# Optimization experiments

Measured on AMD Instinct MI355X. Metric: run time of the kernel, lower is better.

## Reference

```python
import jax, jax.numpy as jnp
import numpy as np

D_MODEL = 2048
N_HEADS = 32
N_KV_HEADS = 8
HEAD_DIM = D_MODEL // N_HEADS
N_REP = N_HEADS // N_KV_HEADS
ROPE_BASE = 10000.0


def _rope_tables(seq_len, dim, dtype):
    inv_freq = 1.0 / (ROPE_BASE ** (jnp.arange(0, dim, 2, dtype=jnp.float32) / dim))
    t = jnp.arange(seq_len, dtype=jnp.float32)
    freqs = jnp.einsum('i,j->ij', t, inv_freq)          # [S, dim/2]
    emb = jnp.concatenate([freqs, freqs], axis=-1)      # [S, dim]
    return jnp.cos(emb).astype(dtype), jnp.sin(emb).astype(dtype)


def _apply_rotation(x, cos, sin):
    # x: [B, H, S, D]; cos/sin: [S, D] broadcast over B,H
    half = x.shape[-1] // 2
    x1, x2 = x[..., :half], x[..., half:]
    rot = jnp.concatenate([-x2, x1], axis=-1)
    return rot * sin + x * cos


def setup_inputs() -> dict:
    key = jax.random.key(0)
    kx, kq, kk, kv, ko = jax.random.split(key, 5)
    B, S = 2, 2048
    scale_in = 1.0 / np.sqrt(D_MODEL)
    x = jax.random.normal(kx, (B, S, D_MODEL), dtype=jnp.float32)
    Wq = jax.random.normal(kq, (N_HEADS * HEAD_DIM, D_MODEL), dtype=jnp.float32) * scale_in
    Wk = jax.random.normal(kk, (N_KV_HEADS * HEAD_DIM, D_MODEL), dtype=jnp.float32) * scale_in
    Wv = jax.random.normal(kv, (N_KV_HEADS * HEAD_DIM, D_MODEL), dtype=jnp.float32) * scale_in
    Wo = jax.random.normal(ko, (D_MODEL, N_HEADS * HEAD_DIM), dtype=jnp.float32) * scale_in
    # additive causal mask, broadcast over batch and heads
    neg = jnp.float32(-1e9)
    causal = jnp.triu(jnp.full((S, S), neg, dtype=jnp.float32), k=1)[None, None]
    return {"x": x, "Wq": Wq, "Wk": Wk, "Wv": Wv, "Wo": Wo, "mask": causal}


def reference(x, Wq, Wk, Wv, Wo, mask):
    B, S, _ = x.shape
    q = (x @ Wq.T).reshape(B, S, N_HEADS, HEAD_DIM).transpose(0, 2, 1, 3)      # [B,H,S,D]
    k = (x @ Wk.T).reshape(B, S, N_KV_HEADS, HEAD_DIM).transpose(0, 2, 1, 3)   # [B,Hkv,S,D]
    v = (x @ Wv.T).reshape(B, S, N_KV_HEADS, HEAD_DIM).transpose(0, 2, 1, 3)
    cos, sin = _rope_tables(S, HEAD_DIM, x.dtype)
    q = _apply_rotation(q, cos, sin)
    k = _apply_rotation(k, cos, sin)
    # repeat_kv: [B,Hkv,S,D] -> [B,Hkv*n_rep,S,D]
    k = jnp.repeat(k, N_REP, axis=1)
    v = jnp.repeat(v, N_REP, axis=1)
    scale = jnp.sqrt(jnp.float32(HEAD_DIM)).astype(x.dtype)
    scores = jnp.einsum('bhqd,bhkd->bhqk', q, k) / scale
    scores = scores + mask
    attn = jax.nn.softmax(scores.astype(jnp.float32), axis=-1).astype(q.dtype)
    out = jnp.einsum('bhqk,bhkd->bhqd', attn, v)
    out = out.transpose(0, 2, 1, 3).reshape(B, S, N_HEADS * HEAD_DIM)
    return out @ Wo.T
```

## Files before the change

kernel.cpp:

```cpp
#include <hip/hip_runtime.h>


typedef __bf16 bf16x8 __attribute__((ext_vector_type(8)));
typedef __bf16 bf16x4 __attribute__((ext_vector_type(4)));
typedef float f32x4 __attribute__((ext_vector_type(4)));

__device__ inline f32x4 mfma16(bf16x8 a, bf16x8 b, f32x4 c) {
    return __builtin_amdgcn_mfma_f32_16x16x32_bf16(a, b, c, 0, 0, 0);
}

__device__ inline void gld16(const __bf16* g, __bf16* l) {
    __builtin_amdgcn_global_load_lds(
        (const __attribute__((address_space(1))) void*)g,
        (__attribute__((address_space(3))) void*)l, 16, 0, 0);
}

__device__ inline bf16x4 pk4(float a, float b, float c, float d) {
    bf16x4 r; r[0] = (__bf16)a; r[1] = (__bf16)b; r[2] = (__bf16)c; r[3] = (__bf16)d;
    return r;
}

#define SCALE_Q 0.18033688011112042f
#define L2IF    0.4152410118609203f
#define INV2PI  0.15915494309189535f

__global__ void cvt4_kernel(const float* __restrict__ x,  const float* __restrict__ wq,
                            const float* __restrict__ wk, const float* __restrict__ wv,
                            __bf16* __restrict__ xb, __bf16* __restrict__ wqkvb)
{
    int i = blockIdx.x * blockDim.x + threadIdx.x;
    const float* src; __bf16* dst;
    if (i < 2097152)      { src = x  + (size_t)i * 4;  dst = xb + (size_t)i * 4; }
    else if (i < 3145728) { int j = i - 2097152; src = wq + (size_t)j * 4; dst = wqkvb + (size_t)j * 4; }
    else if (i < 3407872) { int j = i - 3145728; src = wk + (size_t)j * 4; dst = wqkvb + 4194304 + (size_t)j * 4; }
    else                  { int j = i - 3407872; src = wv + (size_t)j * 4; dst = wqkvb + 5242880 + (size_t)j * 4; }
    float4 f = *(const float4*)src;
    *(bf16x4*)dst = pk4(f.x, f.y, f.z, f.w);
}

__global__ void cvt_kernel(const float* __restrict__ in, __bf16* __restrict__ out, int n4)
{
    int i = blockIdx.x * blockDim.x + threadIdx.x;
    if (i >= n4) return;
    float4 f = ((const float4*)in)[i];
    ((bf16x4*)out)[i] = pk4(f.x, f.y, f.z, f.w);
}

template<bool ROPE, bool OUT_F32>
__global__ __launch_bounds__(512, 2) void gemm256(
    const __bf16* __restrict__ A, const __bf16* __restrict__ Bw,
    void* __restrict__ Cv, int M, int N, int K)
{
    __shared__ __bf16 LA[2][16384];
    __shared__ __bf16 LB[2][16384];
    const int tid  = threadIdx.x;
    const int lane = tid & 63;
    const int w    = tid >> 6;
    const int lm   = lane & 15;
    const int quad = lane >> 4;
    const int wr   = w >> 2;
    const int wc   = w & 3;

    int bx, by;
    {
        int nwg = gridDim.x * gridDim.y;
        int id  = blockIdx.x + gridDim.x * blockIdx.y;
        int q   = nwg >> 3;
        int swz = (id & 7) * q + (id >> 3);
        by = swz / gridDim.x;
        bx = swz - by * gridDim.x;
    }
    const int m0 = by * 256;
    const int n0 = bx * 256;
    const int NT = K >> 6;

    const int srow = tid >> 3;
    const int scol = ((tid & 7) ^ (srow & 7)) * 8;
    const int ldst = tid * 8;
    const __bf16* ga = A  + (size_t)(m0 + srow) * K + scol;
    const __bf16* gb = Bw + (size_t)(n0 + srow) * K + scol;

    auto STA = [&](int bf, int r, int u) {
        gld16(ga + (size_t)r * K + u * 64, &LA[bf][r * 64 + ldst]);
    };
    auto STB = [&](int bf, int r, int u) {
        gld16(gb + (size_t)r * K + u * 64, &LB[bf][r * 64 + ldst]);
    };

    f32x4 acc[8][4];
    #pragma unroll
    for (int i = 0; i < 8; ++i)
        #pragma unroll
        for (int j = 0; j < 4; ++j)
            acc[i][j] = (f32x4){0.f, 0.f, 0.f, 0.f};

    const int axo = (wr * 128 + lm) * 64;
    const int bxo = (wc * 64  + lm) * 64;
    const int ks0 = ((quad * 8)      ^ ((lm & 7) * 8));
    const int ks1 = ((32 + quad * 8) ^ ((lm & 7) * 8));

    STA(0, 0, 0); STA(0, 64, 0); STA(0, 128, 0); STA(0, 192, 0);
    STB(0, 0, 0); STB(0, 64, 0); STB(0, 128, 0); STB(0, 192, 0);
    STA(1, 0, 1); STA(1, 128, 1); STB(1, 0, 1); STA(1, 64, 1); STB(1, 64, 1);
    asm volatile("s_waitcnt vmcnt(5)" ::: "memory");
    __builtin_amdgcn_s_barrier();
    asm volatile("" ::: "memory");

    bf16x8 Af[4][2], Bf[4][2];
    for (int t = 0; t < NT; ++t) {
        const int b = t & 1;
        const __bf16* la = LA[b];
        const __bf16* lb = LB[b];
        #pragma unroll
        for (int mi = 0; mi < 4; ++mi) {
            Af[mi][0] = *(const bf16x8*)(la + axo + mi * 1024 + ks0);
            Af[mi][1] = *(const bf16x8*)(la + axo + mi * 1024 + ks1);
        }
        #pragma unroll
        for (int ni = 0; ni < 2; ++ni) {
            Bf[ni][0] = *(const bf16x8*)(lb + bxo + ni * 1024 + ks0);
            Bf[ni][1] = *(const bf16x8*)(lb + bxo + ni * 1024 + ks1);
        }
        if (t + 1 < NT) { STA(b ^ 1, 192, t + 1); STB(b ^ 1, 128, t + 1); }
        __builtin_amdgcn_s_barrier();
        asm volatile("s_waitcnt lgkmcnt(0)" ::: "memory");
        __builtin_amdgcn_s_setprio(1);
        #pragma unroll
        for (int mi = 0; mi < 4; ++mi)
            #pragma unroll
            for (int ni = 0; ni < 2; ++ni) {
                acc[mi][ni] = mfma16(Af[mi][0], Bf[ni][0], acc[mi][ni]);
                acc[mi][ni] = mfma16(Af[mi][1], Bf[ni][1], acc[mi][ni]);
            }
        __builtin_amdgcn_s_setprio(0);
        __builtin_amdgcn_s_barrier();
        #pragma unroll
        for (int ni = 2; ni < 4; ++ni) {
            Bf[ni][0] = *(const bf16x8*)(lb + bxo + ni * 1024 + ks0);
            Bf[ni][1] = *(const bf16x8*)(lb + bxo + ni * 1024 + ks1);
        }
        if (t + 1 < NT) STB(b ^ 1, 192, t + 1);
        if (t + 2 < NT) STA(b, 0, t + 2);
        __builtin_amdgcn_s_barrier();
        asm volatile("s_waitcnt lgkmcnt(0)" ::: "memory");
        __builtin_amdgcn_s_setprio(1);
        #pragma unroll
        for (int mi = 0; mi < 4; ++mi)
            #pragma unroll
            for (int ni = 2; ni < 4; ++ni) {
                acc[mi][ni] = mfma16(Af[mi][0], Bf[ni][0], acc[mi][ni]);
                acc[mi][ni] = mfma16(Af[mi][1], Bf[ni][1], acc[mi][ni]);
            }
        __builtin_amdgcn_s_setprio(0);
        __builtin_amdgcn_s_barrier();
        #pragma unroll
        for (int mi = 0; mi < 4; ++mi) {
            Af[mi][0] = *(const bf16x8*)(la + axo + (mi + 4) * 1024 + ks0);
            Af[mi][1] = *(const bf16x8*)(la + axo + (mi + 4) * 1024 + ks1);
        }
        if (t + 2 < NT) { STA(b, 128, t + 2); STB(b, 0, t + 2); }
        __builtin_amdgcn_s_barrier();
        asm volatile("s_waitcnt lgkmcnt(0)" ::: "memory");
        __builtin_amdgcn_s_setprio(1);
        #pragma unroll
        for (int mi = 0; mi < 4; ++mi)
            #pragma unroll
            for (int ni = 0; ni < 2; ++ni) {
                acc[mi + 4][ni] = mfma16(Af[mi][0], Bf[ni][0], acc[mi + 4][ni]);
                acc[mi + 4][ni] = mfma16(Af[mi][1], Bf[ni][1], acc[mi + 4][ni]);
            }
        __builtin_amdgcn_s_setprio(0);
        __builtin_amdgcn_s_barrier();
        if (t + 2 < NT) { STA(b, 64, t + 2); STB(b, 64, t + 2); }
        __builtin_amdgcn_s_barrier();
        __builtin_amdgcn_s_setprio(1);
        #pragma unroll
        for (int mi = 0; mi < 4; ++mi)
            #pragma unroll
            for (int ni = 2; ni < 4; ++ni) {
                acc[mi + 4][ni] = mfma16(Af[mi][0], Bf[ni][0], acc[mi + 4][ni]);
                acc[mi + 4][ni] = mfma16(Af[mi][1], Bf[ni][1], acc[mi + 4][ni]);
            }
        __builtin_amdgcn_s_setprio(0);
        if (t < NT - 2)       asm volatile("s_waitcnt vmcnt(5)" ::: "memory");
        else if (t == NT - 2) asm volatile("s_waitcnt vmcnt(0)" ::: "memory");
        __builtin_amdgcn_s_barrier();
        asm volatile("" ::: "memory");
    }

    float sc = 1.0f;
    if (ROPE) {
        const int colbase = n0 + wc * 64;
        const int region  = (colbase < 2048) ? 0 : (colbase < 2560 ? 1 : 2);
        if (region < 2) {
            if (region == 0) sc = SCALE_Q;
            float invr[2];
            invr[0] = exp2f(-(float)lm        * L2IF) * INV2PI;
            invr[1] = exp2f(-(float)(16 + lm) * L2IF) * INV2PI;
            #pragma unroll
            for (int i = 0; i < 8; ++i)
                #pragma unroll
                for (int r = 0; r < 4; ++r) {
                    float tt = (float)((m0 + wr * 128 + i * 16 + quad * 4 + r) & 2047);
                    #pragma unroll
                    for (int jp = 0; jp < 2; ++jp) {
                        float aR = tt * invr[jp];
                        aR -= floorf(aR);
                        float cs = __builtin_amdgcn_cosf(aR);
                        float sn = __builtin_amdgcn_sinf(aR);
                        float x1 = acc[i][jp][r], x2 = acc[i][jp + 2][r];
                        acc[i][jp][r]     = x1 * cs - x2 * sn;
                        acc[i][jp + 2][r] = x2 * cs + x1 * sn;
                    }
                }
        }
    }

    #pragma unroll
    for (int i = 0; i < 8; ++i)
        #pragma unroll
        for (int j = 0; j < 4; ++j)
            #pragma unroll
            for (int r = 0; r < 4; ++r) {
                int row = m0 + wr * 128 + i * 16 + quad * 4 + r;
                int col = n0 + wc * 64 + j * 16 + lm;
                if (OUT_F32)
                    ((float*)Cv)[(size_t)row * N + col] = acc[i][j][r];
                else
                    ((__bf16*)Cv)[(size_t)row * N + col] = (__bf16)(acc[i][j][r] * sc);
            }
}

__global__ __launch_bounds__(512, 2) void gemm_o(
    const __bf16* __restrict__ A, const __bf16* __restrict__ Bw,
    float* __restrict__ C, int M, int N, int K)
{
    __shared__ __bf16 LA[2][16384];
    __shared__ __bf16 LB[2][8192];
    const int tid  = threadIdx.x;
    const int lane = tid & 63;
    const int w    = tid >> 6;
    const int lm   = lane & 15;
    const int quad = lane >> 4;
    const int wr   = w >> 1;
    const int wc   = w & 1;

    int bx, by;
    {
        int id  = blockIdx.x + gridDim.x * blockIdx.y;
        int swz = (id & 7) * 32 + (id >> 3);
        by = swz >> 4;
        bx = swz & 15;
    }
    const int m0 = by * 256;
    const int n0 = bx * 128;
    const int NT = K >> 6;

    const int srow = tid >> 3;
    const int scol = ((tid & 7) ^ (srow & 7)) * 8;
    const int ldst = tid * 8;
    const __bf16* ga = A  + (size_t)(m0 + srow) * K + scol;
    const __bf16* gb = Bw + (size_t)(n0 + srow) * K + scol;

    auto STA = [&](int bf, int r, int u) {
        gld16(ga + (size_t)r * K + u * 64, &LA[bf][r * 64 + ldst]);
    };
    auto STB = [&](int bf, int r, int u) {
        gld16(gb + (size_t)r * K + u * 64, &LB[bf][r * 64 + ldst]);
    };

    f32x4 acc[4][4];
    #pragma unroll
    for (int i = 0; i < 4; ++i)
        #pragma unroll
        for (int j = 0; j < 4; ++j)
            acc[i][j] = (f32x4){0.f, 0.f, 0.f, 0.f};

    const int axo = (wr * 64 + lm) * 64;
    const int bxo = (wc * 64 + lm) * 64;
    const int ks0 = ((quad * 8)      ^ ((lm & 7) * 8));
    const int ks1 = ((32 + quad * 8) ^ ((lm & 7) * 8));

    STA(0, 0, 0); STA(0, 64, 0); STA(0, 128, 0); STA(0, 192, 0);
    STB(0, 0, 0); STB(0, 64, 0);
    STA(1, 0, 1); STA(1, 64, 1); STA(1, 128, 1); STA(1, 192, 1);
    STB(1, 0, 1); STB(1, 64, 1);
    asm volatile("s_waitcnt vmcnt(6)" ::: "memory");
    __builtin_amdgcn_s_barrier();
    asm volatile("" ::: "memory");

    bf16x8 Af[4][2], Bf[4][2];
    for (int t = 0; t < NT; ++t) {
        const int b = t & 1;
        const __bf16* la = LA[b];
        const __bf16* lb = LB[b];
        #pragma unroll
        for (int mi = 0; mi < 2; ++mi) {
            Af[mi][0] = *(const bf16x8*)(la + axo + mi * 1024 + ks0);
            Af[mi][1] = *(const bf16x8*)(la + axo + mi * 1024 + ks1);
        }
        #pragma unroll
        for (int ni = 0; ni < 2; ++ni) {
            Bf[ni][0] = *(const bf16x8*)(lb + bxo + ni * 1024 + ks0);
            Bf[ni][1] = *(const bf16x8*)(lb + bxo + ni * 1024 + ks1);
        }
        __builtin_amdgcn_s_barrier();
        asm volatile("s_waitcnt lgkmcnt(0)" ::: "memory");
        __builtin_amdgcn_s_setprio(1);
        #pragma unroll
        for (int mi = 0; mi < 2; ++mi)
            #pragma unroll
            for (int ni = 0; ni < 2; ++ni) {
                acc[mi][ni] = mfma16(Af[mi][0], Bf[ni][0], acc[mi][ni]);
                acc[mi][ni] = mfma16(Af[mi][1], Bf[ni][1], acc[mi][ni]);
            }
        __builtin_amdgcn_s_setprio(0);
        __builtin_amdgcn_s_barrier();
        #pragma unroll
        for (int ni = 2; ni < 4; ++ni) {
            Bf[ni][0] = *(const bf16x8*)(lb + bxo + ni * 1024 + ks0);
            Bf[ni][1] = *(const bf16x8*)(lb + bxo + ni * 1024 + ks1);
        }
        __builtin_amdgcn_s_barrier();
        asm volatile("s_waitcnt lgkmcnt(0)" ::: "memory");
        __builtin_amdgcn_s_setprio(1);
        #pragma unroll
        for (int mi = 0; mi < 2; ++mi)
            #pragma unroll
            for (int ni = 2; ni < 4; ++ni) {
                acc[mi][ni] = mfma16(Af[mi][0], Bf[ni][0], acc[mi][ni]);
                acc[mi][ni] = mfma16(Af[mi][1], Bf[ni][1], acc[mi][ni]);
            }
        __builtin_amdgcn_s_setprio(0);
        __builtin_amdgcn_s_barrier();
        #pragma unroll
        for (int mi = 2; mi < 4; ++mi) {
            Af[mi][0] = *(const bf16x8*)(la + axo + mi * 1024 + ks0);
            Af[mi][1] = *(const bf16x8*)(la + axo + mi * 1024 + ks1);
        }
        if (t + 2 < NT) { STB(b, 0, t + 2); STB(b, 64, t + 2); }
        __builtin_amdgcn_s_barrier();
        asm volatile("s_waitcnt lgkmcnt(0)" ::: "memory");
        __builtin_amdgcn_s_setprio(1);
        #pragma unroll
        for (int mi = 2; mi < 4; ++mi)
            #pragma unroll
            for (int ni = 0; ni < 2; ++ni) {
                acc[mi][ni] = mfma16(Af[mi][0], Bf[ni][0], acc[mi][ni]);
                acc[mi][ni] = mfma16(Af[mi][1], Bf[ni][1], acc[mi][ni]);
            }
        __builtin_amdgcn_s_setprio(0);
        __builtin_amdgcn_s_barrier();
        if (t + 2 < NT) {
            STA(b, 0, t + 2); STA(b, 64, t + 2);
            STA(b, 128, t + 2); STA(b, 192, t + 2);
        }
        __builtin_amdgcn_s_setprio(1);
        #pragma unroll
        for (int mi = 2; mi < 4; ++mi)
            #pragma unroll
            for (int ni = 2; ni < 4; ++ni) {
                acc[mi][ni] = mfma16(Af[mi][0], Bf[ni][0], acc[mi][ni]);
                acc[mi][ni] = mfma16(Af[mi][1], Bf[ni][1], acc[mi][ni]);
            }
        __builtin_amdgcn_s_setprio(0);
        if (t < NT - 2) asm volatile("s_waitcnt vmcnt(6)" ::: "memory");
        else            asm volatile("s_waitcnt vmcnt(0)" ::: "memory");
        __builtin_amdgcn_s_barrier();
        asm volatile("" ::: "memory");
    }

    #pragma unroll
    for (int i = 0; i < 4; ++i)
        #pragma unroll
        for (int j = 0; j < 4; ++j)
            #pragma unroll
            for (int r = 0; r < 4; ++r) {
                int row = m0 + wr * 64 + i * 16 + quad * 4 + r;
                int col = n0 + wc * 64 + j * 16 + lm;
                C[(size_t)row * N + col] = acc[i][j][r];
            }
}

__global__ __launch_bounds__(256) void transpose_kernel(
    const __bf16* __restrict__ in, __bf16* __restrict__ out, int rowstride)
{
    __shared__ __bf16 T[64][72];
    const int t0 = blockIdx.x * 64;
    const int d0 = blockIdx.y * 64;
    const int r = threadIdx.x >> 2, c = (threadIdx.x & 3) * 16;
    *(int4*)&T[r][c]     = *(const int4*)(in + (size_t)(t0 + r) * rowstride + d0 + c);
    *(int4*)&T[r][c + 8] = *(const int4*)(in + (size_t)(t0 + r) * rowstride + d0 + c + 8);
    __syncthreads();
    bf16x8 o0, o1;
    #pragma unroll
    for (int i = 0; i < 8; ++i) { o0[i] = T[c + i][r]; o1[i] = T[c + 8 + i][r]; }
    *(bf16x8*)(out + (size_t)(d0 + r) * 4096 + t0 + c)     = o0;
    *(bf16x8*)(out + (size_t)(d0 + r) * 4096 + t0 + c + 8) = o1;
}

#define RS  64
#define PKS 64

__device__ inline void attn_tile(
    const bf16x8 (&qf)[2], f32x4 (&oacc)[4], float& l,
    int qbase, int k0, int w, int lm, int quad,
    const __bf16* Ks, const __bf16* Vs, __bf16* Ptw)
{
    const int kb0 = (quad ^ (lm & 7)) * 8;
    const int kb1 = ((quad + 4) ^ (lm & 7)) * 8;
    f32x4 st[4];
    #pragma unroll
    for (int n = 0; n < 4; ++n)
        st[n] = (f32x4){0.f, 0.f, 0.f, 0.f};

    #pragma unroll
    for (int n = 0; n < 4; ++n) {
        bf16x8 kf0 = *(const bf16x8*)&Ks[(n * 16 + lm) * RS + kb0];
        bf16x8 kf1 = *(const bf16x8*)&Ks[(n * 16 + lm) * RS + kb1];
        st[n] = mfma16(kf0, qf[0], st[n]);
        st[n] = mfma16(kf1, qf[1], st[n]);
    }

    const int qi = qbase + w * 16 + lm;
    const bool any_mask = (k0 + 63 > qbase + w * 16);
    #pragma unroll
    for (int n = 0; n < 4; ++n) {
        const int kv0 = k0 + n * 16 + quad * 4;
        float e0, e1, e2, e3;
        if (any_mask) {
            e0 = (kv0     > qi) ? 0.f : __builtin_amdgcn_exp2f(st[n][0]);
            e1 = (kv0 + 1 > qi) ? 0.f : __builtin_amdgcn_exp2f(st[n][1]);
            e2 = (kv0 + 2 > qi) ? 0.f : __builtin_amdgcn_exp2f(st[n][2]);
            e3 = (kv0 + 3 > qi) ? 0.f : __builtin_amdgcn_exp2f(st[n][3]);
        } else {
            e0 = __builtin_amdgcn_exp2f(st[n][0]); e1 = __builtin_amdgcn_exp2f(st[n][1]);
            e2 = __builtin_amdgcn_exp2f(st[n][2]); e3 = __builtin_amdgcn_exp2f(st[n][3]);
        }
        l += (e0 + e1) + (e2 + e3);
        *(bf16x4*)&Ptw[lm * PKS + ((n * 4 + quad) ^ ((lm & 7) << 1)) * 4] =
            pk4(e0, e1, e2, e3);
    }

    bf16x8 pf0 = *(const bf16x8*)&Ptw[lm * PKS + kb0];
    bf16x8 pf1 = *(const bf16x8*)&Ptw[lm * PKS + kb1];
    #pragma unroll
    for (int dt = 0; dt < 4; ++dt) {
        bf16x8 vf0 = *(const bf16x8*)&Vs[(dt * 16 + lm) * RS + kb0];
        bf16x8 vf1 = *(const bf16x8*)&Vs[(dt * 16 + lm) * RS + kb1];
        oacc[dt] = mfma16(vf0, pf0, oacc[dt]);
        oacc[dt] = mfma16(vf1, pf1, oacc[dt]);
    }
}

__device__ inline void attn_tile2(
    const bf16x8 (&qfA)[2], const bf16x8 (&qfB)[2],
    f32x4 (&oA)[4], f32x4 (&oB)[4], float& lA, float& lB,
    int qbA, int k0, int w, int lm, int quad,
    const __bf16* Ks, const __bf16* Vs, __bf16* PtA, __bf16* PtB)
{
    const int kb0 = (quad ^ (lm & 7)) * 8;
    const int kb1 = ((quad + 4) ^ (lm & 7)) * 8;
    f32x4 stA[4], stB[4];
    #pragma unroll
    for (int n = 0; n < 4; ++n) {
        stA[n] = (f32x4){0.f, 0.f, 0.f, 0.f};
        stB[n] = (f32x4){0.f, 0.f, 0.f, 0.f};
    }

    #pragma unroll
    for (int n = 0; n < 4; ++n) {
        bf16x8 kf0 = *(const bf16x8*)&Ks[(n * 16 + lm) * RS + kb0];
        bf16x8 kf1 = *(const bf16x8*)&Ks[(n * 16 + lm) * RS + kb1];
        stB[n] = mfma16(kf0, qfB[0], stB[n]);
        stB[n] = mfma16(kf1, qfB[1], stB[n]);
        stA[n] = mfma16(kf0, qfA[0], stA[n]);
        stA[n] = mfma16(kf1, qfA[1], stA[n]);
    }

    #pragma unroll
    for (int n = 0; n < 4; ++n) {
        float e0 = __builtin_amdgcn_exp2f(stB[n][0]);
        float e1 = __builtin_amdgcn_exp2f(stB[n][1]);
        float e2 = __builtin_amdgcn_exp2f(stB[n][2]);
        float e3 = __builtin_amdgcn_exp2f(stB[n][3]);
        lB += (e0 + e1) + (e2 + e3);
        *(bf16x4*)&PtB[lm * PKS + ((n * 4 + quad) ^ ((lm & 7) << 1)) * 4] =
            pk4(e0, e1, e2, e3);
    }

    const int qiA = qbA + w * 16 + lm;
    const bool maskA = (k0 + 63 > qbA + w * 16);
    #pragma unroll
    for (int n = 0; n < 4; ++n) {
        const int kv0 = k0 + n * 16 + quad * 4;
        float e0, e1, e2, e3;
        if (maskA) {
            e0 = (kv0     > qiA) ? 0.f : __builtin_amdgcn_exp2f(stA[n][0]);
            e1 = (kv0 + 1 > qiA) ? 0.f : __builtin_amdgcn_exp2f(stA[n][1]);
            e2 = (kv0 + 2 > qiA) ? 0.f : __builtin_amdgcn_exp2f(stA[n][2]);
            e3 = (kv0 + 3 > qiA) ? 0.f : __builtin_amdgcn_exp2f(stA[n][3]);
        } else {
            e0 = __builtin_amdgcn_exp2f(stA[n][0]); e1 = __builtin_amdgcn_exp2f(stA[n][1]);
            e2 = __builtin_amdgcn_exp2f(stA[n][2]); e3 = __builtin_amdgcn_exp2f(stA[n][3]);
        }
        lA += (e0 + e1) + (e2 + e3);
        *(bf16x4*)&PtA[lm * PKS + ((n * 4 + quad) ^ ((lm & 7) << 1)) * 4] =
            pk4(e0, e1, e2, e3);
    }

    bf16x8 pB0 = *(const bf16x8*)&PtB[lm * PKS + kb0];
    bf16x8 pB1 = *(const bf16x8*)&PtB[lm * PKS + kb1];
    bf16x8 pA0 = *(const bf16x8*)&PtA[lm * PKS + kb0];
    bf16x8 pA1 = *(const bf16x8*)&PtA[lm * PKS + kb1];
    #pragma unroll
    for (int dt = 0; dt < 4; ++dt) {
        bf16x8 vf0 = *(const bf16x8*)&Vs[(dt * 16 + lm) * RS + kb0];
        bf16x8 vf1 = *(const bf16x8*)&Vs[(dt * 16 + lm) * RS + kb1];
        oB[dt] = mfma16(vf0, pB0, oB[dt]);
        oB[dt] = mfma16(vf1, pB1, oB[dt]);
        oA[dt] = mfma16(vf0, pA0, oA[dt]);
        oA[dt] = mfma16(vf1, pA1, oA[dt]);
    }
}

__device__ inline void attn_epilogue(
    f32x4 (&oacc)[4], float l,
    int qbase, int w, int lm, int quad, int b, int h, __bf16* o)
{
    float ls = l;
    ls += __shfl_xor(ls, 16);
    ls += __shfl_xor(ls, 32);
    float rinv = 1.0f / ls;
    const size_t rowbase = (size_t)(b * 2048 + qbase + w * 16 + lm) * 2048 + h * 64;
    #pragma unroll
    for (int dt = 0; dt < 4; ++dt) {
        *(bf16x4*)(o + rowbase + dt * 16 + quad * 4) =
            pk4(oacc[dt][0] * rinv, oacc[dt][1] * rinv,
                oacc[dt][2] * rinv, oacc[dt][3] * rinv);
    }
}

__global__ __launch_bounds__(512, 4) void attn_kernel(
    const __bf16* __restrict__ qkv, const __bf16* __restrict__ vt,
    __bf16* __restrict__ o)
{
    __shared__ __bf16 Ks[2][64 * RS];
    __shared__ __bf16 Vs[2][64 * RS];
    __shared__ __bf16 Pt[8][2][16 * PKS];
    const int tid  = threadIdx.x;
    const int w    = tid >> 6;
    const int lane = tid & 63;
    const int lm   = lane & 15;
    const int quad = lane >> 4;
    const int p = blockIdx.x, h = blockIdx.y, b = blockIdx.z;
    const int kvh = h >> 2;
    const int qbA = p * 128, qbB = (15 - p) * 128;
    const int ntA = 2 * p + 2, ntB = 32 - 2 * p;
    __bf16* PtwB = &Pt[w][0][0];
    __bf16* PtwA = &Pt[w][1][0];

    bf16x8 qfA[2], qfB[2];
    #pragma unroll
    for (int kh = 0; kh < 2; ++kh) {
        qfA[kh] = *(const bf16x8*)(qkv + (size_t)(b * 2048 + qbA + w * 16 + lm) * 3072
                                      + h * 64 + kh * 32 + quad * 8);
        qfB[kh] = *(const bf16x8*)(qkv + (size_t)(b * 2048 + qbB + w * 16 + lm) * 3072
                                      + h * 64 + kh * 32 + quad * 8);
    }

    f32x4 oA[4], oB[4];
    float lA = 0.f, lB = 0.f;
    #pragma unroll
    for (int j = 0; j < 4; ++j) {
        oA[j] = (f32x4){0.f, 0.f, 0.f, 0.f};
        oB[j] = (f32x4){0.f, 0.f, 0.f, 0.f};
    }

    const int srow = tid >> 3;
    const int scg  = (tid & 7) * 8;
    const int scl  = (((tid & 7) ^ (srow & 7))) * 8;
    const __bf16* kbase = qkv + (size_t)(b * 2048) * 3072 + 2048 + kvh * 64;
    const __bf16* vbase = vt  + (size_t)(kvh * 64 + srow) * 4096 + b * 2048;

    int4 kr0, vr0;
    kr0 = *(const int4*)(kbase + (size_t)srow * 3072 + scg);
    vr0 = *(const int4*)(vbase + scg);

    for (int kt = 0; kt < ntB; ++kt) {
        const int c = kt & 1;
        const int k0 = kt * 64;
        *(int4*)&Ks[c][srow * RS + scl] = kr0;
        *(int4*)&Vs[c][srow * RS + scl] = vr0;
        if (kt + 1 < ntB) {
            kr0 = *(const int4*)(kbase + (size_t)(k0 + 64 + srow) * 3072 + scg);
            vr0 = *(const int4*)(vbase + k0 + 64 + scg);
        }
        __syncthreads();
        if (kt < ntA)
            attn_tile2(qfA, qfB, oA, oB, lA, lB, qbA, k0, w, lm, quad,
                       Ks[c], Vs[c], PtwA, PtwB);
        else
            attn_tile(qfB, oB, lB, qbB, k0, w, lm, quad, Ks[c], Vs[c], PtwB);
    }

    attn_epilogue(oA, lA, qbA, w, lm, quad, b, h, o);
    attn_epilogue(oB, lB, qbB, w, lm, quad, b, h, o);
}

extern "C" void kernel_launch(void* const* d_in, const int* in_sizes, int n_in,
                              void* d_out, int out_size, void* d_ws, size_t ws_size,
                              hipStream_t stream)
{
    const float* x  = (const float*)d_in[0];
    const float* Wq = (const float*)d_in[1];
    const float* Wk = (const float*)d_in[2];
    const float* Wv = (const float*)d_in[3];
    const float* Wo = (const float*)d_in[4];

    const size_t Mi = 1u << 20;
    char* ob = (char*)d_out;
    __bf16* xb    = (__bf16*)ob;
    __bf16* wqkvb = (__bf16*)(ob + 16 * Mi);
    __bf16* vt    = (__bf16*)(ob + 28 * Mi);
    char* ws = (char*)d_ws;
    __bf16* qkvc = (__bf16*)ws;
    __bf16* aws  = (__bf16*)(ws + 24 * Mi);
    __bf16* wob  = (__bf16*)ws;

    dim3 blk(256);
    cvt4_kernel<<<14336, blk, 0, stream>>>(x, Wq, Wk, Wv, xb, wqkvb);
    gemm256<true, false><<<dim3(12, 16), dim3(512), 0, stream>>>(xb, wqkvb, qkvc, 4096, 3072, 2048);
    transpose_kernel<<<dim3(64, 8), blk, 0, stream>>>(qkvc + 2560, vt, 3072);
    attn_kernel<<<dim3(8, 32, 2), dim3(512), 0, stream>>>(qkvc, vt, aws);
    cvt_kernel<<<4096, blk, 0, stream>>>(Wo, wob, 1048576);
    gemm_o<<<dim3(16, 16), dim3(512), 0, stream>>>(aws, wob, (float*)d_out, 4096, 2048, 2048);
}
```

Before: 292.7 us.

## Retile QKV GEMM to 256x192 tiles with permuted weight rows for RoPE

The QKV projection GEMM changes from a 12x16 grid of 256x256 tiles to a 16x16 grid of 256x192 tiles, giving 256 workgroups to better fill the 256 CUs. Each wave now computes a 64x96 sub-tile, and the LDS load pipeline is restructured so all A and B stores for a stage are issued together. To keep RoPE pairs (d, d+32) inside one wave's registers, the Q and K weight rows are permuted during bf16 conversion. The epilogue then un-permutes columns when writing. This costs extra index arithmetic and a less regular global write pattern in the epilogue.

```diff
diff --git a/kernel.cpp b/kernel.cpp
--- a/kernel.cpp
+++ b/kernel.cpp
@@ -24,6 +24,12 @@
 #define L2IF    0.4152410118609203f
 #define INV2PI  0.15915494309189535f
 
+__device__ inline int permrow(int n) {
+    int nod = n & 63;
+    int hj = ((nod >> 5) & 1) | (((nod >> 4) & 1) << 1);
+    return (n & ~63) | (hj << 4) | (nod & 15);
+}
+
 __global__ void cvt4_kernel(const float* __restrict__ x,  const float* __restrict__ wq,
                             const float* __restrict__ wk, const float* __restrict__ wv,
                             __bf16* __restrict__ xb, __bf16* __restrict__ wqkvb)
@@ -31,8 +37,16 @@
     int i = blockIdx.x * blockDim.x + threadIdx.x;
     const float* src; __bf16* dst;
     if (i < 2097152)      { src = x  + (size_t)i * 4;  dst = xb + (size_t)i * 4; }
-    else if (i < 3145728) { int j = i - 2097152; src = wq + (size_t)j * 4; dst = wqkvb + (size_t)j * 4; }
-    else if (i < 3407872) { int j = i - 3145728; src = wk + (size_t)j * 4; dst = wqkvb + 4194304 + (size_t)j * 4; }
+    else if (i < 3145728) {
+        int j = i - 2097152; int n = j >> 9; int off = (j & 511) * 4;
+        src = wq + (size_t)j * 4;
+        dst = wqkvb + (size_t)permrow(n) * 2048 + off;
+    }
+    else if (i < 3407872) {
+        int j = i - 3145728; int n = j >> 9; int off = (j & 511) * 4;
+        src = wk + (size_t)j * 4;
+        dst = wqkvb + 4194304 + (size_t)permrow(n) * 2048 + off;
+    }
     else                  { int j = i - 3407872; src = wv + (size_t)j * 4; dst = wqkvb + 5242880 + (size_t)j * 4; }
     float4 f = *(const float4*)src;
     *(bf16x4*)dst = pk4(f.x, f.y, f.z, f.w);
@@ -46,32 +60,29 @@
     ((bf16x4*)out)[i] = pk4(f.x, f.y, f.z, f.w);
 }
 
-template<bool ROPE, bool OUT_F32>
-__global__ __launch_bounds__(512, 2) void gemm256(
+__global__ __launch_bounds__(512, 2) void gemm_qkv(
     const __bf16* __restrict__ A, const __bf16* __restrict__ Bw,
-    void* __restrict__ Cv, int M, int N, int K)
+    __bf16* __restrict__ C, int M, int N, int K)
 {
     __shared__ __bf16 LA[2][16384];
-    __shared__ __bf16 LB[2][16384];
+    __shared__ __bf16 LB[2][12288];
     const int tid  = threadIdx.x;
     const int lane = tid & 63;
     const int w    = tid >> 6;
     const int lm   = lane & 15;
     const int quad = lane >> 4;
-    const int wr   = w >> 2;
-    const int wc   = w & 3;
+    const int wr   = w >> 1;
+    const int wc   = w & 1;
 
     int bx, by;
     {
-        int nwg = gridDim.x * gridDim.y;
         int id  = blockIdx.x + gridDim.x * blockIdx.y;
-        int q   = nwg >> 3;
-        int swz = (id & 7) * q + (id >> 3);
-        by = swz / gridDim.x;
-        bx = swz - by * gridDim.x;
+        int swz = (id & 7) * 32 + (id >> 3);
+        by = swz >> 4;
+        bx = swz & 15;
     }
     const int m0 = by * 256;
-    const int n0 = bx * 256;
+    const int n0 = bx * 192;
     const int NT = K >> 6;
 
     const int srow = tid >> 3;
@@ -87,148 +98,151 @@
         gld16(gb + (size_t)r * K + u * 64, &LB[bf][r * 64 + ldst]);
     };
 
-    f32x4 acc[8][4];
-    #pragma unroll
-    for (int i = 0; i < 8; ++i)
-        #pragma unroll
-        for (int j = 0; j < 4; ++j)
+    f32x4 acc[4][6];
+    #pragma unroll
+    for (int i = 0; i < 4; ++i)
+        #pragma unroll
+        for (int j = 0; j < 6; ++j)
             acc[i][j] = (f32x4){0.f, 0.f, 0.f, 0.f};
 
-    const int axo = (wr * 128 + lm) * 64;
-    const int bxo = (wc * 64  + lm) * 64;
+    const int axo = (wr * 64 + lm) * 64;
+    const int bxo = (wc * 96 + lm) * 64;
     const int ks0 = ((quad * 8)      ^ ((lm & 7) * 8));
     const int ks1 = ((32 + quad * 8) ^ ((lm & 7) * 8));
 
     STA(0, 0, 0); STA(0, 64, 0); STA(0, 128, 0); STA(0, 192, 0);
-    STB(0, 0, 0); STB(0, 64, 0); STB(0, 128, 0); STB(0, 192, 0);
-    STA(1, 0, 1); STA(1, 128, 1); STB(1, 0, 1); STA(1, 64, 1); STB(1, 64, 1);
-    asm volatile("s_waitcnt vmcnt(5)" ::: "memory");
+    STB(0, 0, 0); STB(0, 64, 0); STB(0, 128, 0);
+    STA(1, 0, 1); STA(1, 64, 1); STA(1, 128, 1); STA(1, 192, 1);
+    STB(1, 0, 1); STB(1, 64, 1); STB(1, 128, 1);
+    asm volatile("s_waitcnt vmcnt(7)" ::: "memory");
     __builtin_amdgcn_s_barrier();
     asm volatile("" ::: "memory");
 
-    bf16x8 Af[4][2], Bf[4][2];
+    bf16x8 Af[2][2], B1[3][2], B2[3][2];
     for (int t = 0; t < NT; ++t) {
         const int b = t & 1;
         const __bf16* la = LA[b];
         const __bf16* lb = LB[b];
         #pragma unroll
-        for (int mi = 0; mi < 4; ++mi) {
+        for (int mi = 0; mi < 2; ++mi) {
             Af[mi][0] = *(const bf16x8*)(la + axo + mi * 1024 + ks0);
             Af[mi][1] = *(const bf16x8*)(la + axo + mi * 1024 + ks1);
         }
         #pragma unroll
-        for (int ni = 0; ni < 2; ++ni) {
-            Bf[ni][0] = *(const bf16x8*)(lb + bxo + ni * 1024 + ks0);
-            Bf[ni][1] = *(const bf16x8*)(lb + bxo + ni * 1024 + ks1);
-        }
-        if (t + 1 < NT) { STA(b ^ 1, 192, t + 1); STB(b ^ 1, 128, t + 1); }
+        for (int ni = 0; ni < 3; ++ni) {
+            B1[ni][0] = *(const bf16x8*)(lb + bxo + ni * 1024 + ks0);
+            B1[ni][1] = *(const bf16x8*)(lb + bxo + ni * 1024 + ks1);
+        }
         __builtin_amdgcn_s_barrier();
         asm volatile("s_waitcnt lgkmcnt(0)" ::: "memory");
         __builtin_amdgcn_s_setprio(1);
         #pragma unroll
-        for (int mi = 0; mi < 4; ++mi)
-            #pragma unroll
-            for (int ni = 0; ni < 2; ++ni) {
-                acc[mi][ni] = mfma16(Af[mi][0], Bf[ni][0], acc[mi][ni]);
-                acc[mi][ni] = mfma16(Af[mi][1], Bf[ni][1], acc[mi][ni]);
-            }
-        __builtin_amdgcn_s_setprio(0);
-        __builtin_amdgcn_s_barrier();
-        #pragma unroll
-        for (int ni = 2; ni < 4; ++ni) {
-            Bf[ni][0] = *(const bf16x8*)(lb + bxo + ni * 1024 + ks0);
-            Bf[ni][1] = *(const bf16x8*)(lb + bxo + ni * 1024 + ks1);
-        }
-        if (t + 1 < NT) STB(b ^ 1, 192, t + 1);
-        if (t + 2 < NT) STA(b, 0, t + 2);
+        for (int mi = 0; mi < 2; ++mi)
+            #pragma unroll
+            for (int ni = 0; ni < 3; ++ni) {
+                acc[mi][ni] = mfma16(Af[mi][0], B1[ni][0], acc[mi][ni]);
+                acc[mi][ni] = mfma16(Af[mi][1], B1[ni][1], acc[mi][ni]);
+            }
+        __builtin_amdgcn_s_setprio(0);
+        __builtin_amdgcn_s_barrier();
+        #pragma unroll
+        for (int ni = 0; ni < 3; ++ni) {
+            B2[ni][0] = *(const bf16x8*)(lb + bxo + (ni + 3) * 1024 + ks0);
+            B2[ni][1] = *(const bf16x8*)(lb + bxo + (ni + 3) * 1024 + ks1);
+        }
         __builtin_amdgcn_s_barrier();
         asm volatile("s_waitcnt lgkmcnt(0)" ::: "memory");
         __builtin_amdgcn_s_setprio(1);
         #pragma unroll
-        for (int mi = 0; mi < 4; ++mi)
-            #pragma unroll
-            for (int ni = 2; ni < 4; ++ni) {
-                acc[mi][ni] = mfma16(Af[mi][0], Bf[ni][0], acc[mi][ni]);
-                acc[mi][ni] = mfma16(Af[mi][1], Bf[ni][1], acc[mi][ni]);
-            }
-        __builtin_amdgcn_s_setprio(0);
-        __builtin_amdgcn_s_barrier();
-        #pragma unroll
-        for (int mi = 0; mi < 4; ++mi) {
-            Af[mi][0] = *(const bf16x8*)(la + axo + (mi + 4) * 1024 + ks0);
-            Af[mi][1] = *(const bf16x8*)(la + axo + (mi + 4) * 1024 + ks1);
-        }
-        if (t + 2 < NT) { STA(b, 128, t + 2); STB(b, 0, t + 2); }
+        for (int mi = 0; mi < 2; ++mi)
+            #pragma unroll
+            for (int ni = 0; ni < 3; ++ni) {
+                acc[mi][ni + 3] = mfma16(Af[mi][0], B2[ni][0], acc[mi][ni + 3]);
+                acc[mi][ni + 3] = mfma16(Af[mi][1], B2[ni][1], acc[mi][ni + 3]);
+            }
+        __builtin_amdgcn_s_setprio(0);
+        __builtin_amdgcn_s_barrier();
+        #pragma unroll
+        for (int mi = 0; mi < 2; ++mi) {
+            Af[mi][0] = *(const bf16x8*)(la + axo + (mi + 2) * 1024 + ks0);
+            Af[mi][1] = *(const bf16x8*)(la + axo + (mi + 2) * 1024 + ks1);
+        }
+        if (t + 2 < NT) { STB(b, 0, t + 2); STB(b, 64, t + 2); STB(b, 128, t + 2); }
         __builtin_amdgcn_s_barrier();
         asm volatile("s_waitcnt lgkmcnt(0)" ::: "memory");
         __builtin_amdgcn_s_setprio(1);
         #pragma unroll
-        for (int mi = 0; mi < 4; ++mi)
-            #pragma unroll
-            for (int ni = 0; ni < 2; ++ni) {
-                acc[mi + 4][ni] = mfma16(Af[mi][0], Bf[ni][0], acc[mi + 4][ni]);
-                acc[mi + 4][ni] = mfma16(Af[mi][1], Bf[ni][1], acc[mi + 4][ni]);
-            }
-        __builtin_amdgcn_s_setprio(0);
-        __builtin_amdgcn_s_barrier();
-        if (t + 2 < NT) { STA(b, 64, t + 2); STB(b, 64, t + 2); }
-        __builtin_amdgcn_s_barrier();
-        __builtin_amdgcn_s_setprio(1);
-        #pragma unroll
-        for (int mi = 0; mi < 4; ++mi)
-            #pragma unroll
-            for (int ni = 2; ni < 4; ++ni) {
-                acc[mi + 4][ni] = mfma16(Af[mi][0], Bf[ni][0], acc[mi + 4][ni]);
-                acc[mi + 4][ni] = mfma16(Af[mi][1], Bf[ni][1], acc[mi + 4][ni]);
-            }
-        __builtin_amdgcn_s_setprio(0);
-        if (t < NT - 2)       asm volatile("s_waitcnt vmcnt(5)" ::: "memory");
-        else if (t == NT - 2) asm volatile("s_waitcnt vmcnt(0)" ::: "memory");
+        for (int mi = 0; mi < 2; ++mi)
+            #pragma unroll
+            for (int ni = 0; ni < 3; ++ni) {
+                acc[mi + 2][ni] = mfma16(Af[mi][0], B1[ni][0], acc[mi + 2][ni]);
+                acc[mi + 2][ni] = mfma16(Af[mi][1], B1[ni][1], acc[mi + 2][ni]);
+            }
+        __builtin_amdgcn_s_setprio(0);
+        __builtin_amdgcn_s_barrier();
+        if (t + 2 < NT) {
+            STA(b, 0, t + 2); STA(b, 64, t + 2);
+            STA(b, 128, t + 2); STA(b, 192, t + 2);
+        }
+        __builtin_amdgcn_s_setprio(1);
+        #pragma unroll
+        for (int mi = 0; mi < 2; ++mi)
+            #pragma unroll
+            for (int ni = 0; ni < 3; ++ni) {
+                acc[mi + 2][ni + 3] = mfma16(Af[mi][0], B2[ni][0], acc[mi + 2][ni + 3]);
+                acc[mi + 2][ni + 3] = mfma16(Af[mi][1], B2[ni][1], acc[mi + 2][ni + 3]);
+            }
+        __builtin_amdgcn_s_setprio(0);
+        if (t < NT - 2) asm volatile("s_waitcnt vmcnt(7)" ::: "memory");
+        else            asm volatile("s_waitcnt vmcnt(0)" ::: "memory");
         __builtin_amdgcn_s_barrier();
         asm volatile("" ::: "memory");
     }
 
-    float sc = 1.0f;
-    if (ROPE) {
-        const int colbase = n0 + wc * 64;
-        const int region  = (colbase < 2048) ? 0 : (colbase < 2560 ? 1 : 2);
-        if (region < 2) {
-            if (region == 0) sc = SCALE_Q;
-            float invr[2];
-            invr[0] = exp2f(-(float)lm        * L2IF) * INV2PI;
-            invr[1] = exp2f(-(float)(16 + lm) * L2IF) * INV2PI;
-            #pragma unroll
-            for (int i = 0; i < 8; ++i)
+    {
+        float invr[2];
+        invr[0] = exp2f(-(float)lm        * L2IF) * INV2PI;
+        invr[1] = exp2f(-(float)(16 + lm) * L2IF) * INV2PI;
+        #pragma unroll
+        for (int jp = 0; jp < 3; ++jp) {
+            const int jlo = jp * 2;
+            const int pcb = n0 + wc * 96 + jlo * 16;
+            if (pcb >= 2560) continue;
+            const int hj = (pcb >> 4) & 3;
+            const float fr = invr[hj >> 1];
+            #pragma unroll
+            for (int i = 0; i < 4; ++i)
                 #pragma unroll
                 for (int r = 0; r < 4; ++r) {
-                    float tt = (float)((m0 + wr * 128 + i * 16 + quad * 4 + r) & 2047);
-                    #pragma unroll
-                    for (int jp = 0; jp < 2; ++jp) {
-                        float aR = tt * invr[jp];
-                        aR -= floorf(aR);
-                        float cs = __builtin_amdgcn_cosf(aR);
-                        float sn = __builtin_amdgcn_sinf(aR);
-                        float x1 = acc[i][jp][r], x2 = acc[i][jp + 2][r];
-                        acc[i][jp][r]     = x1 * cs - x2 * sn;
-                        acc[i][jp + 2][r] = x2 * cs + x1 * sn;
-                    }
+                    float tt = (float)((m0 + wr * 64 + i * 16 + quad * 4 + r) & 2047);
+                    float aR = tt * fr;
+                    aR -= floorf(aR);
+                    float cs = __builtin_amdgcn_cosf(aR);
+                    float sn = __builtin_amdgcn_sinf(aR);
+                    float x1 = acc[i][jlo][r], x2 = acc[i][jlo + 1][r];
+                    acc[i][jlo][r]     = x1 * cs - x2 * sn;
+                    acc[i][jlo + 1][r] = x2 * cs + x1 * sn;
                 }
         }
     }
 
     #pragma unroll
-    for (int i = 0; i < 8; ++i)
-        #pragma unroll
-        for (int j = 0; j < 4; ++j)
+    for (int j = 0; j < 6; ++j) {
+        const int pcb = n0 + wc * 96 + j * 16;
+        int colb; float sc;
+        if (pcb < 2560) {
+            const int hj = (pcb >> 4) & 3;
+            colb = (pcb & ~63) | ((hj & 1) << 5) | ((hj >> 1) << 4);
+            sc = (pcb < 2048) ? SCALE_Q : 1.0f;
+        } else { colb = pcb; sc = 1.0f; }
+        #pragma unroll
+        for (int i = 0; i < 4; ++i)
             #pragma unroll
             for (int r = 0; r < 4; ++r) {
-                int row = m0 + wr * 128 + i * 16 + quad * 4 + r;
-                int col = n0 + wc * 64 + j * 16 + lm;
-                if (OUT_F32)
-                    ((float*)Cv)[(size_t)row * N + col] = acc[i][j][r];
-                else
-                    ((__bf16*)Cv)[(size_t)row * N + col] = (__bf16)(acc[i][j][r] * sc);
-            }
+                int row = m0 + wr * 64 + i * 16 + quad * 4 + r;
+                C[(size_t)row * N + colb + lm] = (__bf16)(acc[i][j][r] * sc);
+            }
+    }
 }
 
 __global__ __launch_bounds__(512, 2) void gemm_o(
@@ -630,7 +644,7 @@
 
     dim3 blk(256);
     cvt4_kernel<<<14336, blk, 0, stream>>>(x, Wq, Wk, Wv, xb, wqkvb);
-    gemm256<true, false><<<dim3(12, 16), dim3(512), 0, stream>>>(xb, wqkvb, qkvc, 4096, 3072, 2048);
+    gemm_qkv<<<dim3(16, 16), dim3(512), 0, stream>>>(xb, wqkvb, qkvc, 4096, 3072, 2048);
     transpose_kernel<<<dim3(64, 8), blk, 0, stream>>>(qkvc + 2560, vt, 3072);
     attn_kernel<<<dim3(8, 32, 2), dim3(512), 0, stream>>>(qkvc, vt, aws);
     cvt_kernel<<<4096, blk, 0, stream>>>(Wo, wob, 1048576);
```

Result: faster. 281.7 us (-3.8%).
